# Performance work log

Measured on AMD Instinct MI355X. Metric: run time of the kernel, lower is better.

## Reference

```python
import jax, jax.numpy as jnp
import numpy as np

B, N, C = 2048, 4096, 1024
UNITS, RANK = 4096, 512


def _orth(key, shape):
    a = jax.random.normal(key, shape, dtype=jnp.float32)
    q, r = jnp.linalg.qr(a if shape[0] >= shape[1] else a.T)
    q = q * jnp.sign(jnp.diagonal(r))[None, :]
    return q if shape[0] >= shape[1] else q.T


def setup_inputs() -> dict:
    key = jax.random.key(0)
    k1, k2, k3, k4, k5, k6 = jax.random.split(key, 6)
    inputs = jax.random.normal(k1, (B, N), dtype=jnp.float32)
    context = jax.random.normal(k2, (B, C), dtype=jnp.float32)
    U = _orth(k3, (N, RANK))
    V = _orth(k4, (UNITS, RANK))
    W = _orth(k5, (C, RANK))
    # SingularValueInitializer stand-in: positive values scaled like glorot singular values
    S = jnp.abs(jax.random.normal(k6, (RANK,), dtype=jnp.float32)) * jnp.sqrt(2.0 / (N + UNITS))
    bias = jnp.zeros((UNITS,), dtype=jnp.float32)
    return {"inputs": inputs, "context": context, "U": U, "S": S, "V": V, "W": W, "bias": bias}


def reference(inputs, context, U, S, V, W, bias):
    # s_b = S + context @ W  -> per-batch singular values [B, R]
    s = S[None, :] + context @ W
    # Original: kernel_b = U diag(s_b) V^T; out_b = x_b @ kernel_b.
    # Associativity: out = ((x @ U) * s) @ V^T  -- identical math, no [B,N,M] intermediate.
    xu = inputs @ U                      # [B, R]
    out = (xu * s) @ V.T                 # [B, UNITS]
    out = out + bias[None, :]
    return jax.nn.relu(out)
```

## Files before the change

kernel.cpp:

```cpp
#include <hip/hip_runtime.h>
#include <hip/hip_bf16.h>

typedef __attribute__((ext_vector_type(8))) __bf16 bf16x8;
typedef __attribute__((ext_vector_type(4))) float f32x4;
typedef __attribute__((ext_vector_type(8))) unsigned short ushort8;
typedef __attribute__((ext_vector_type(4))) unsigned short ushort4v;

__device__ __forceinline__ unsigned short f2bf(float f) {
  unsigned u = __builtin_bit_cast(unsigned, f);
  u += 0x7FFFu + ((u >> 16) & 1u);
  return (unsigned short)(u >> 16);
}

__device__ __forceinline__ void gload_lds16(const void* g, void* l) {
  __builtin_amdgcn_global_load_lds(
      (const __attribute__((address_space(1))) void*)g,
      (__attribute__((address_space(3))) void*)l, 16, 0, 0);
}

__device__ __forceinline__ void barrier_fence() {
  __builtin_amdgcn_s_barrier();
  asm volatile("" ::: "memory");
}

template <int N>
__device__ __forceinline__ void waitvm() {
  if constexpr (N == 0)       asm volatile("s_waitcnt vmcnt(0)" ::: "memory");
  else if constexpr (N == 8)  asm volatile("s_waitcnt vmcnt(8)" ::: "memory");
  else if constexpr (N == 16) asm volatile("s_waitcnt vmcnt(16)" ::: "memory");
}

__global__ __launch_bounds__(256) void prep_kernel(
    const float* __restrict__ U, unsigned short* __restrict__ Ut,
    const float* __restrict__ W, unsigned short* __restrict__ Wt,
    const float* __restrict__ V, unsigned short* __restrict__ Vb,
    const float* __restrict__ inp, unsigned short* __restrict__ inb,
    const float* __restrict__ ctx, unsigned short* __restrict__ ctxb) {
  __shared__ float tile[32][33];
  const int b = blockIdx.x;
  const int tid = threadIdx.x;
  if (b < 2560) {
    const float* src;
    unsigned short* dst;
    int rows, cols, bx, by;
    if (b < 2048) {
      src = U; dst = Ut; rows = 4096; cols = 512;
      bx = (b & 15) * 32; by = (b >> 4) * 32;
    } else {
      int bb = b - 2048;
      src = W; dst = Wt; rows = 1024; cols = 512;
      bx = (bb & 15) * 32; by = (bb >> 4) * 32;
    }
    const int tx = tid & 31, ty = tid >> 5;
    for (int i = ty; i < 32; i += 8)
      tile[i][tx] = src[(size_t)(by + i) * cols + bx + tx];
    __syncthreads();
    for (int i = ty; i < 32; i += 8)
      dst[(size_t)(bx + i) * rows + by + tx] = f2bf(tile[tx][i]);
  } else {
    const float* src;
    unsigned short* dst;
    size_t i;
    if (b < 3584)      { src = V;   dst = Vb;   i = (size_t)(b - 2560) * 256 + tid; }
    else if (b < 7680) { src = inp; dst = inb;  i = (size_t)(b - 3584) * 256 + tid; }
    else               { src = ctx; dst = ctxb; i = (size_t)(b - 7680) * 256 + tid; }
    const float4* s4 = reinterpret_cast<const float4*>(src) + 2 * i;
    float4 a = s4[0], c = s4[1];
    ushort8 o;
    o[0] = f2bf(a.x); o[1] = f2bf(a.y); o[2] = f2bf(a.z); o[3] = f2bf(a.w);
    o[4] = f2bf(c.x); o[5] = f2bf(c.y); o[6] = f2bf(c.z); o[7] = f2bf(c.w);
    *(reinterpret_cast<ushort8*>(dst) + i) = o;
  }
}

template <int FM, int FN, int EPI, int DEPTH>
__device__ __forceinline__ void gemm_core(
    const unsigned short* __restrict__ A, const unsigned short* __restrict__ Bt,
    int N, int lda, int kchunk, const float* __restrict__ e0,
    float* __restrict__ outf, int nwg, int bid) {
  constexpr int BM = 32 * FM, BN = 32 * FN, BK = 64;
  constexpr int AI = FM, BI = FN;
  constexpr int ISS = AI + BI;
  __shared__ unsigned short lds[DEPTH][(BM + BN) * BK];

  const int tid = threadIdx.x;
  const int wid = tid >> 6;
  const int lane = tid & 63;
  const int wr = wid >> 1, wc = wid & 1;

  const int swz = (bid & 7) * (nwg >> 3) + (bid >> 3);
  const int nbn = N / BN;
  const int brow = (swz / nbn) * BM;
  const int bcol = (swz % nbn) * BN;

  f32x4 zero = {0.f, 0.f, 0.f, 0.f};
  f32x4 acc[FM][FN];
#pragma unroll
  for (int m = 0; m < FM; ++m)
#pragma unroll
    for (int n = 0; n < FN; ++n) acc[m][n] = zero;

  const int lr = lane >> 3;
  const int swzc = ((lane & 7) ^ lr) * 8;
  const unsigned short* Agh = A + (size_t)(brow + wid * (BM / 4) + lr) * lda + swzc;
  const unsigned short* Bgh = Bt + (size_t)(bcol + wid * (BN / 4) + lr) * lda + swzc;

  const int frow = lane & 15;
  const int fhi = lane >> 4;

  const int nsteps = kchunk / BK;

  auto stage = [&](int b, int kofs) {
    unsigned short* AsW = lds[b] + wid * (BM / 4) * 64;
#pragma unroll
    for (int i = 0; i < AI; ++i)
      gload_lds16(Agh + kofs + (size_t)(8 * i) * lda, AsW + i * 512);
    unsigned short* BsW = lds[b] + BM * BK + wid * (BN / 4) * 64;
#pragma unroll
    for (int i = 0; i < BI; ++i)
      gload_lds16(Bgh + kofs + (size_t)(8 * i) * lda, BsW + i * 512);
  };

  auto compute = [&](int cur) {
    const unsigned short* As = lds[cur];
    const unsigned short* Bs = lds[cur] + BM * BK;
#pragma unroll
    for (int ks = 0; ks < 2; ++ks) {
      bf16x8 af[FM], bg[FN];
#pragma unroll
      for (int m = 0; m < FM; ++m) {
        int row = wr * FM * 16 + m * 16 + frow;
        int pc = (ks * 4 + fhi) ^ (row & 7);
        af[m] = *reinterpret_cast<const bf16x8*>(As + row * 64 + pc * 8);
      }
#pragma unroll
      for (int n = 0; n < FN; ++n) {
        int row = wc * FN * 16 + n * 16 + frow;
        int pc = (ks * 4 + fhi) ^ (row & 7);
        bg[n] = *reinterpret_cast<const bf16x8*>(Bs + row * 64 + pc * 8);
      }
#pragma unroll
      for (int m = 0; m < FM; ++m)
#pragma unroll
        for (int n = 0; n < FN; ++n)
          acc[m][n] = __builtin_amdgcn_mfma_f32_16x16x32_bf16(af[m], bg[n],
                                                              acc[m][n], 0, 0, 0);
    }
  };

#pragma unroll
  for (int d = 0; d < DEPTH; ++d) stage(d, d * BK);

  int cur = 0;
  for (int t = 0; t < nsteps; ++t) {
    const int ahead = nsteps - 1 - t;
    if (ahead >= DEPTH - 1)
      waitvm<(DEPTH - 1) * ISS>();
    else
      waitvm<0>();
    barrier_fence();
    compute(cur);
    if (t + 1 < nsteps) {
      asm volatile("s_waitcnt lgkmcnt(0)" ::: "memory");
      barrier_fence();
      if (t + DEPTH < nsteps) stage(cur, (t + DEPTH) * BK);
    }
    cur = (cur + 1 == DEPTH) ? 0 : cur + 1;
  }

#pragma unroll
  for (int m = 0; m < FM; ++m) {
    int gr0 = brow + wr * FM * 16 + m * 16 + fhi * 4;
#pragma unroll
    for (int n = 0; n < FN; ++n) {
      int gc = bcol + wc * FN * 16 + n * 16 + frow;
#pragma unroll
      for (int j = 0; j < 4; ++j) {
        size_t idx = (size_t)(gr0 + j) * N + gc;
        float v = acc[m][n][j];
        if constexpr (EPI == 2) {
          v += e0[gc];
          outf[idx] = v > 0.f ? v : 0.f;
        } else {
          outf[idx] = v;
        }
      }
    }
  }
}

__global__ __launch_bounds__(256) void gemm01_kernel(
    const unsigned short* __restrict__ inb, const unsigned short* __restrict__ Ut,
    const unsigned short* __restrict__ ctxb, const unsigned short* __restrict__ Wt,
    float* __restrict__ p0, float* __restrict__ p1) {
  const int bid = (int)blockIdx.x;
  constexpr size_t MN = (size_t)2048 * 512;
  if (bid < 256) {
    const int split = bid >> 6;
    gemm_core<4, 4, 3, 2>(inb + (size_t)split * 1024,
                          Ut + (size_t)split * 1024,
                          512, 4096, 1024, nullptr,
                          p1 + split * MN, 64, bid & 63);
  } else {
    const int sb = bid - 256;
    const int split = sb >> 6;
    gemm_core<4, 4, 3, 2>(ctxb + (size_t)split * 512,
                          Wt + (size_t)split * 512,
                          512, 1024, 512, nullptr,
                          p0 + split * MN, 64, sb & 63);
  }
}

__global__ __launch_bounds__(256) void gemm2_kernel(
    const unsigned short* __restrict__ xus, const unsigned short* __restrict__ Vb,
    const float* __restrict__ bias, float* __restrict__ out) {
  gemm_core<4, 4, 2, 2>(xus, Vb, 4096, 512, 512, bias, out, 512,
                        (int)blockIdx.x);
}

__global__ void reduce_mul_kernel(const float* __restrict__ p1,
                                  const float* __restrict__ p0,
                                  const float* __restrict__ Svec,
                                  unsigned short* __restrict__ xus, int MN) {
  int i = blockIdx.x * blockDim.x + threadIdx.x;
  size_t base = (size_t)i * 4;
  if (base >= (size_t)MN) return;
  float4 a = *reinterpret_cast<const float4*>(p1 + base);
  float4 b = *reinterpret_cast<const float4*>(p1 + (size_t)MN + base);
  float4 c = *reinterpret_cast<const float4*>(p1 + 2 * (size_t)MN + base);
  float4 d = *reinterpret_cast<const float4*>(p1 + 3 * (size_t)MN + base);
  float4 s0 = *reinterpret_cast<const float4*>(p0 + base);
  float4 s1 = *reinterpret_cast<const float4*>(p0 + (size_t)MN + base);
  float4 sv = *reinterpret_cast<const float4*>(Svec + (base & 511));
  float4 xu, s;
  xu.x = (a.x + b.x) + (c.x + d.x);  s.x = s0.x + s1.x + sv.x;
  xu.y = (a.y + b.y) + (c.y + d.y);  s.y = s0.y + s1.y + sv.y;
  xu.z = (a.z + b.z) + (c.z + d.z);  s.z = s0.z + s1.z + sv.z;
  xu.w = (a.w + b.w) + (c.w + d.w);  s.w = s0.w + s1.w + sv.w;
  ushort4v o;
  o[0] = f2bf(xu.x * s.x);
  o[1] = f2bf(xu.y * s.y);
  o[2] = f2bf(xu.z * s.z);
  o[3] = f2bf(xu.w * s.w);
  *reinterpret_cast<ushort4v*>(xus + base) = o;
}

extern "C" void kernel_launch(void* const* d_in, const int* in_sizes, int n_in,
                              void* d_out, int out_size, void* d_ws, size_t ws_size,
                              hipStream_t stream) {
  constexpr int Bm = 2048, Nn = 4096, Cc = 1024, UU = 4096, RR = 512;
  const float* inputs  = (const float*)d_in[0];
  const float* context = (const float*)d_in[1];
  const float* U       = (const float*)d_in[2];
  const float* S       = (const float*)d_in[3];
  const float* V       = (const float*)d_in[4];
  const float* W       = (const float*)d_in[5];
  const float* bias    = (const float*)d_in[6];
  float* out = (float*)d_out;

  char* p = (char*)d_ws;
  unsigned short* Ut   = (unsigned short*)p; p += (size_t)RR * Nn * 2;
  unsigned short* Wt   = (unsigned short*)p; p += (size_t)RR * Cc * 2;
  unsigned short* Vb   = (unsigned short*)p; p += (size_t)UU * RR * 2;
  unsigned short* inb  = (unsigned short*)p; p += (size_t)Bm * Nn * 2;
  unsigned short* ctxb = (unsigned short*)p; p += (size_t)Bm * Cc * 2;
  float*          p0   = (float*)p;          p += (size_t)2 * Bm * RR * 4;
  float*          p1   = (float*)p;          p += (size_t)4 * Bm * RR * 4;
  unsigned short* xus  = (unsigned short*)p; p += (size_t)Bm * RR * 2;

  prep_kernel<<<8704, 256, 0, stream>>>(U, Ut, W, Wt, V, Vb, inputs, inb,
                                        context, ctxb);

  gemm01_kernel<<<384, 256, 0, stream>>>(inb, Ut, ctxb, Wt, p0, p1);

  reduce_mul_kernel<<<Bm * RR / 4 / 256, 256, 0, stream>>>(p1, p0, S, xus, Bm * RR);

  gemm2_kernel<<<512, 256, 0, stream>>>(xus, Vb, bias, out);
}
```

Baseline: 54.20 us.

## Fuse fp32-to-bf16 conversion of activations into the first GEMM's A-tile load

Removes the separate bf16 conversion pass over inputs and context, so the prep kernel no longer writes and the GEMM no longer rereads the converted copies. A new GEMM core loads the fp32 A tiles into registers, converts them to bf16 and stores them to a swizzled LDS layout, while B still goes directly from global memory to LDS. A-loads are software-pipelined two steps ahead. The trade-off is twice the A-side global bytes per tile, extra VALU conversion work and register pressure inside the GEMM, plus a full vmcnt(0) wait each step.

```diff
diff --git a/kernel.cpp b/kernel.cpp
--- a/kernel.cpp
+++ b/kernel.cpp
@@ -25,17 +25,14 @@
 
 template <int N>
 __device__ __forceinline__ void waitvm() {
-  if constexpr (N == 0)       asm volatile("s_waitcnt vmcnt(0)" ::: "memory");
-  else if constexpr (N == 8)  asm volatile("s_waitcnt vmcnt(8)" ::: "memory");
-  else if constexpr (N == 16) asm volatile("s_waitcnt vmcnt(16)" ::: "memory");
+  if constexpr (N == 0)      asm volatile("s_waitcnt vmcnt(0)" ::: "memory");
+  else if constexpr (N == 8) asm volatile("s_waitcnt vmcnt(8)" ::: "memory");
 }
 
 __global__ __launch_bounds__(256) void prep_kernel(
     const float* __restrict__ U, unsigned short* __restrict__ Ut,
     const float* __restrict__ W, unsigned short* __restrict__ Wt,
-    const float* __restrict__ V, unsigned short* __restrict__ Vb,
-    const float* __restrict__ inp, unsigned short* __restrict__ inb,
-    const float* __restrict__ ctx, unsigned short* __restrict__ ctxb) {
+    const float* __restrict__ V, unsigned short* __restrict__ Vb) {
   __shared__ float tile[32][33];
   const int b = blockIdx.x;
   const int tid = threadIdx.x;
@@ -58,18 +55,13 @@
     for (int i = ty; i < 32; i += 8)
       dst[(size_t)(bx + i) * rows + by + tx] = f2bf(tile[tx][i]);
   } else {
-    const float* src;
-    unsigned short* dst;
-    size_t i;
-    if (b < 3584)      { src = V;   dst = Vb;   i = (size_t)(b - 2560) * 256 + tid; }
-    else if (b < 7680) { src = inp; dst = inb;  i = (size_t)(b - 3584) * 256 + tid; }
-    else               { src = ctx; dst = ctxb; i = (size_t)(b - 7680) * 256 + tid; }
-    const float4* s4 = reinterpret_cast<const float4*>(src) + 2 * i;
+    const size_t i = (size_t)(b - 2560) * 256 + tid;
+    const float4* s4 = reinterpret_cast<const float4*>(V) + 2 * i;
     float4 a = s4[0], c = s4[1];
     ushort8 o;
     o[0] = f2bf(a.x); o[1] = f2bf(a.y); o[2] = f2bf(a.z); o[3] = f2bf(a.w);
     o[4] = f2bf(c.x); o[5] = f2bf(c.y); o[6] = f2bf(c.z); o[7] = f2bf(c.w);
-    *(reinterpret_cast<ushort8*>(dst) + i) = o;
+    *(reinterpret_cast<ushort8*>(Vb) + i) = o;
   }
 }
 
@@ -189,25 +181,144 @@
   }
 }
 
+__device__ __forceinline__ void gemm_core_f32a(
+    const float* __restrict__ A, const unsigned short* __restrict__ Bt,
+    int lda, int kchunk, float* __restrict__ outf, int nwg, int bid) {
+  constexpr int N = 512;
+  constexpr int BM = 128, BN = 128, BK = 64;
+  __shared__ unsigned short lds[2][(BM + BN) * BK];
+
+  const int tid = threadIdx.x;
+  const int wid = tid >> 6;
+  const int lane = tid & 63;
+  const int wr = wid >> 1, wc = wid & 1;
+
+  const int swz = (bid & 7) * (nwg >> 3) + (bid >> 3);
+  const int nbn = N / BN;
+  const int brow = (swz / nbn) * BM;
+  const int bcol = (swz % nbn) * BN;
+
+  f32x4 zero = {0.f, 0.f, 0.f, 0.f};
+  f32x4 acc[4][4];
+#pragma unroll
+  for (int m = 0; m < 4; ++m)
+#pragma unroll
+    for (int n = 0; n < 4; ++n) acc[m][n] = zero;
+
+  const int lr = lane >> 3;
+  const int lc = lane & 7;
+  const int swzc = (lc ^ lr) * 8;
+  const float* Agf = A + (size_t)(brow + wid * 32 + lr) * lda + swzc;
+  const unsigned short* Bgh = Bt + (size_t)(bcol + wid * 32 + lr) * lda + swzc;
+
+  const int frow = lane & 15;
+  const int fhi = lane >> 4;
+
+  const int nsteps = kchunk / BK;
+
+  float4 areg[4][2];
+  auto aload = [&](int kofs) {
+#pragma unroll
+    for (int i = 0; i < 4; ++i) {
+      const float* s = Agf + kofs + (size_t)(8 * i) * lda;
+      areg[i][0] = *reinterpret_cast<const float4*>(s);
+      areg[i][1] = *reinterpret_cast<const float4*>(s + 4);
+    }
+  };
+  auto awrite = [&](int b) {
+    unsigned short* AsW = lds[b] + wid * 2048 + lane * 8;
+#pragma unroll
+    for (int i = 0; i < 4; ++i) {
+      float4 x = areg[i][0], y = areg[i][1];
+      ushort8 o;
+      o[0] = f2bf(x.x); o[1] = f2bf(x.y); o[2] = f2bf(x.z); o[3] = f2bf(x.w);
+      o[4] = f2bf(y.x); o[5] = f2bf(y.y); o[6] = f2bf(y.z); o[7] = f2bf(y.w);
+      *reinterpret_cast<ushort8*>(AsW + i * 512) = o;
+    }
+  };
+  auto bload = [&](int b, int kofs) {
+    unsigned short* BsW = lds[b] + BM * BK + wid * 2048;
+#pragma unroll
+    for (int i = 0; i < 4; ++i)
+      gload_lds16(Bgh + kofs + (size_t)(8 * i) * lda, BsW + i * 512);
+  };
+
+  auto compute = [&](int cur) {
+    const unsigned short* As = lds[cur];
+    const unsigned short* Bs = lds[cur] + BM * BK;
+#pragma unroll
+    for (int ks = 0; ks < 2; ++ks) {
+      bf16x8 af[4], bg[4];
+#pragma unroll
+      for (int m = 0; m < 4; ++m) {
+        int row = wr * 64 + m * 16 + frow;
+        int pc = (ks * 4 + fhi) ^ (row & 7);
+        af[m] = *reinterpret_cast<const bf16x8*>(As + row * 64 + pc * 8);
+      }
+#pragma unroll
+      for (int n = 0; n < 4; ++n) {
+        int row = wc * 64 + n * 16 + frow;
+        int pc = (ks * 4 + fhi) ^ (row & 7);
+        bg[n] = *reinterpret_cast<const bf16x8*>(Bs + row * 64 + pc * 8);
+      }
+#pragma unroll
+      for (int m = 0; m < 4; ++m)
+#pragma unroll
+        for (int n = 0; n < 4; ++n)
+          acc[m][n] = __builtin_amdgcn_mfma_f32_16x16x32_bf16(af[m], bg[n],
+                                                              acc[m][n], 0, 0, 0);
+    }
+  };
+
+  aload(0);
+  bload(0, 0);
+  waitvm<0>();
+  awrite(0);
+  aload(BK);
+  asm volatile("s_waitcnt lgkmcnt(0)" ::: "memory");
+  barrier_fence();
+
+  for (int t = 0; t < nsteps; ++t) {
+    const int cur = t & 1;
+    if (t + 1 < nsteps) bload(cur ^ 1, (t + 1) * BK);
+    compute(cur);
+    if (t + 1 < nsteps) {
+      waitvm<0>();
+      awrite(cur ^ 1);
+      if (t + 2 < nsteps) aload((t + 2) * BK);
+      asm volatile("s_waitcnt lgkmcnt(0)" ::: "memory");
+      barrier_fence();
+    }
+  }
+
+#pragma unroll
+  for (int m = 0; m < 4; ++m) {
+    int gr0 = brow + wr * 64 + m * 16 + fhi * 4;
+#pragma unroll
+    for (int n = 0; n < 4; ++n) {
+      int gc = bcol + wc * 64 + n * 16 + frow;
+#pragma unroll
+      for (int j = 0; j < 4; ++j)
+        outf[(size_t)(gr0 + j) * N + gc] = acc[m][n][j];
+    }
+  }
+}
+
 __global__ __launch_bounds__(256) void gemm01_kernel(
-    const unsigned short* __restrict__ inb, const unsigned short* __restrict__ Ut,
-    const unsigned short* __restrict__ ctxb, const unsigned short* __restrict__ Wt,
+    const float* __restrict__ inp, const unsigned short* __restrict__ Ut,
+    const float* __restrict__ ctx, const unsigned short* __restrict__ Wt,
     float* __restrict__ p0, float* __restrict__ p1) {
   const int bid = (int)blockIdx.x;
   constexpr size_t MN = (size_t)2048 * 512;
   if (bid < 256) {
     const int split = bid >> 6;
-    gemm_core<4, 4, 3, 2>(inb + (size_t)split * 1024,
-                          Ut + (size_t)split * 1024,
-                          512, 4096, 1024, nullptr,
-                          p1 + split * MN, 64, bid & 63);
+    gemm_core_f32a(inp + (size_t)split * 1024, Ut + (size_t)split * 1024,
+                   4096, 1024, p1 + split * MN, 64, bid & 63);
   } else {
     const int sb = bid - 256;
     const int split = sb >> 6;
-    gemm_core<4, 4, 3, 2>(ctxb + (size_t)split * 512,
-                          Wt + (size_t)split * 512,
-                          512, 1024, 512, nullptr,
-                          p0 + split * MN, 64, sb & 63);
+    gemm_core_f32a(ctx + (size_t)split * 512, Wt + (size_t)split * 512,
+                   1024, 512, p0 + split * MN, 64, sb & 63);
   }
 }
 
@@ -262,16 +373,13 @@
   unsigned short* Ut   = (unsigned short*)p; p += (size_t)RR * Nn * 2;
   unsigned short* Wt   = (unsigned short*)p; p += (size_t)RR * Cc * 2;
   unsigned short* Vb   = (unsigned short*)p; p += (size_t)UU * RR * 2;
-  unsigned short* inb  = (unsigned short*)p; p += (size_t)Bm * Nn * 2;
-  unsigned short* ctxb = (unsigned short*)p; p += (size_t)Bm * Cc * 2;
   float*          p0   = (float*)p;          p += (size_t)2 * Bm * RR * 4;
   float*          p1   = (float*)p;          p += (size_t)4 * Bm * RR * 4;
   unsigned short* xus  = (unsigned short*)p; p += (size_t)Bm * RR * 2;
 
-  prep_kernel<<<8704, 256, 0, stream>>>(U, Ut, W, Wt, V, Vb, inputs, inb,
-                                        context, ctxb);
-
-  gemm01_kernel<<<384, 256, 0, stream>>>(inb, Ut, ctxb, Wt, p0, p1);
+  prep_kernel<<<3584, 256, 0, stream>>>(U, Ut, W, Wt, V, Vb);
+
+  gemm01_kernel<<<384, 256, 0, stream>>>(inputs, Ut, context, Wt, p0, p1);
 
   reduce_mul_kernel<<<Bm * RR / 4 / 256, 256, 0, stream>>>(p1, p0, S, xus, Bm * RR);
 
```

Result: faster. 52.10 us (-3.9%).

## Raise split-K to 8 for x@U GEMM and use column-major tile mapping in output GEMM

Applied to the files above, without the earlier changes.

The x@U GEMM is split eight ways along K instead of four, so each block covers a 512-wide K chunk and gemm01 launches 640 blocks instead of 384. This gives better CU occupancy on a machine with 256 CUs and a balanced per-block load. The cost is twice the fp32 partial traffic written by gemm01 and read back in reduce_mul. The output GEMM also switches to a column-major block mapping, which changes L2 reuse of the V tiles versus the activation tiles.

```diff
diff --git a/kernel.cpp b/kernel.cpp
--- a/kernel.cpp
+++ b/kernel.cpp
@@ -25,9 +25,8 @@
 
 template <int N>
 __device__ __forceinline__ void waitvm() {
-  if constexpr (N == 0)       asm volatile("s_waitcnt vmcnt(0)" ::: "memory");
-  else if constexpr (N == 8)  asm volatile("s_waitcnt vmcnt(8)" ::: "memory");
-  else if constexpr (N == 16) asm volatile("s_waitcnt vmcnt(16)" ::: "memory");
+  if constexpr (N == 0)      asm volatile("s_waitcnt vmcnt(0)" ::: "memory");
+  else if constexpr (N == 8) asm volatile("s_waitcnt vmcnt(8)" ::: "memory");
 }
 
 __global__ __launch_bounds__(256) void prep_kernel(
@@ -73,7 +72,7 @@
   }
 }
 
-template <int FM, int FN, int EPI, int DEPTH>
+template <int FM, int FN, int EPI, int DEPTH, bool COLMAP>
 __device__ __forceinline__ void gemm_core(
     const unsigned short* __restrict__ A, const unsigned short* __restrict__ Bt,
     int N, int lda, int kchunk, const float* __restrict__ e0,
@@ -90,8 +89,15 @@
 
   const int swz = (bid & 7) * (nwg >> 3) + (bid >> 3);
   const int nbn = N / BN;
-  const int brow = (swz / nbn) * BM;
-  const int bcol = (swz % nbn) * BN;
+  int brow, bcol;
+  if constexpr (COLMAP) {
+    const int nbm = nwg / nbn;
+    brow = (swz % nbm) * BM;
+    bcol = (swz / nbm) * BN;
+  } else {
+    brow = (swz / nbn) * BM;
+    bcol = (swz % nbn) * BN;
+  }
 
   f32x4 zero = {0.f, 0.f, 0.f, 0.f};
   f32x4 acc[FM][FN];
@@ -195,27 +201,29 @@
     float* __restrict__ p0, float* __restrict__ p1) {
   const int bid = (int)blockIdx.x;
   constexpr size_t MN = (size_t)2048 * 512;
-  if (bid < 256) {
+  const unsigned short *A, *Bt;
+  int lda, lbid;
+  float* outp;
+  if (bid < 512) {
     const int split = bid >> 6;
-    gemm_core<4, 4, 3, 2>(inb + (size_t)split * 1024,
-                          Ut + (size_t)split * 1024,
-                          512, 4096, 1024, nullptr,
-                          p1 + split * MN, 64, bid & 63);
+    A = inb + (size_t)split * 512;
+    Bt = Ut + (size_t)split * 512;
+    lda = 4096; outp = p1 + split * MN; lbid = bid & 63;
   } else {
-    const int sb = bid - 256;
+    const int sb = bid - 512;
     const int split = sb >> 6;
-    gemm_core<4, 4, 3, 2>(ctxb + (size_t)split * 512,
-                          Wt + (size_t)split * 512,
-                          512, 1024, 512, nullptr,
-                          p0 + split * MN, 64, sb & 63);
-  }
+    A = ctxb + (size_t)split * 512;
+    Bt = Wt + (size_t)split * 512;
+    lda = 1024; outp = p0 + split * MN; lbid = sb & 63;
+  }
+  gemm_core<4, 4, 3, 2, false>(A, Bt, 512, lda, 512, nullptr, outp, 64, lbid);
 }
 
 __global__ __launch_bounds__(256) void gemm2_kernel(
     const unsigned short* __restrict__ xus, const unsigned short* __restrict__ Vb,
     const float* __restrict__ bias, float* __restrict__ out) {
-  gemm_core<4, 4, 2, 2>(xus, Vb, 4096, 512, 512, bias, out, 512,
-                        (int)blockIdx.x);
+  gemm_core<4, 4, 2, 2, true>(xus, Vb, 4096, 512, 512, bias, out, 512,
+                              (int)blockIdx.x);
 }
 
 __global__ void reduce_mul_kernel(const float* __restrict__ p1,
@@ -225,18 +233,20 @@
   int i = blockIdx.x * blockDim.x + threadIdx.x;
   size_t base = (size_t)i * 4;
   if (base >= (size_t)MN) return;
-  float4 a = *reinterpret_cast<const float4*>(p1 + base);
-  float4 b = *reinterpret_cast<const float4*>(p1 + (size_t)MN + base);
-  float4 c = *reinterpret_cast<const float4*>(p1 + 2 * (size_t)MN + base);
-  float4 d = *reinterpret_cast<const float4*>(p1 + 3 * (size_t)MN + base);
+  float4 xu = {0.f, 0.f, 0.f, 0.f};
+#pragma unroll
+  for (int k = 0; k < 8; ++k) {
+    float4 a = *reinterpret_cast<const float4*>(p1 + (size_t)k * MN + base);
+    xu.x += a.x; xu.y += a.y; xu.z += a.z; xu.w += a.w;
+  }
   float4 s0 = *reinterpret_cast<const float4*>(p0 + base);
   float4 s1 = *reinterpret_cast<const float4*>(p0 + (size_t)MN + base);
   float4 sv = *reinterpret_cast<const float4*>(Svec + (base & 511));
-  float4 xu, s;
-  xu.x = (a.x + b.x) + (c.x + d.x);  s.x = s0.x + s1.x + sv.x;
-  xu.y = (a.y + b.y) + (c.y + d.y);  s.y = s0.y + s1.y + sv.y;
-  xu.z = (a.z + b.z) + (c.z + d.z);  s.z = s0.z + s1.z + sv.z;
-  xu.w = (a.w + b.w) + (c.w + d.w);  s.w = s0.w + s1.w + sv.w;
+  float4 s;
+  s.x = s0.x + s1.x + sv.x;
+  s.y = s0.y + s1.y + sv.y;
+  s.z = s0.z + s1.z + sv.z;
+  s.w = s0.w + s1.w + sv.w;
   ushort4v o;
   o[0] = f2bf(xu.x * s.x);
   o[1] = f2bf(xu.y * s.y);
@@ -265,13 +275,13 @@
   unsigned short* inb  = (unsigned short*)p; p += (size_t)Bm * Nn * 2;
   unsigned short* ctxb = (unsigned short*)p; p += (size_t)Bm * Cc * 2;
   float*          p0   = (float*)p;          p += (size_t)2 * Bm * RR * 4;
-  float*          p1   = (float*)p;          p += (size_t)4 * Bm * RR * 4;
+  float*          p1   = (float*)p;          p += (size_t)8 * Bm * RR * 4;
   unsigned short* xus  = (unsigned short*)p; p += (size_t)Bm * RR * 2;
 
   prep_kernel<<<8704, 256, 0, stream>>>(U, Ut, W, Wt, V, Vb, inputs, inb,
                                         context, ctxb);
 
-  gemm01_kernel<<<384, 256, 0, stream>>>(inb, Ut, ctxb, Wt, p0, p1);
+  gemm01_kernel<<<640, 256, 0, stream>>>(inb, Ut, ctxb, Wt, p0, p1);
 
   reduce_mul_kernel<<<Bm * RR / 4 / 256, 256, 0, stream>>>(p1, p0, S, xus, Bm * RR);
 
```

Result: slower. 58.04 us (+7.1%).
